# Performance work log

Hardware: AMD Instinct MI355X
Metric: run time of the kernel (lower is better)

## Reference

```python
import jax, jax.numpy as jnp
import numpy as np

N_NODES = 50000
N_EDGES = 800000
HIDDEN = 128
EDGE_DIM = 16
N_HEADS = 8
HEAD_DIM = HIDDEN // N_HEADS
SCALE = 1.0 / np.sqrt(HEAD_DIM).astype(np.float32)
LN_EPS = 1e-5


def setup_inputs() -> dict:
    key = jax.random.key(0)
    ks = jax.random.split(key, 24)
    s = 0.02

    def w(k, shape):
        return jax.random.normal(k, shape, dtype=jnp.float32) * s

    inp = {
        "node_features": jax.random.normal(ks[0], (N_NODES, HIDDEN), dtype=jnp.float32),
        "edge_index": jax.random.randint(ks[1], (2, N_EDGES), 0, N_NODES, dtype=jnp.int32),
        "edge_features": jax.random.normal(ks[2], (N_EDGES, EDGE_DIM), dtype=jnp.float32),
        # projections stored as [in, out] (y = x @ W + b)
        "Wq": w(ks[3], (HIDDEN, HIDDEN)), "bq": jnp.zeros((HIDDEN,), jnp.float32),
        "Wk": w(ks[4], (HIDDEN, HIDDEN)), "bk": jnp.zeros((HIDDEN,), jnp.float32),
        "Wv": w(ks[5], (HIDDEN, HIDDEN)), "bv": jnp.zeros((HIDDEN,), jnp.float32),
        "Wb1": w(ks[6], (EDGE_DIM, N_HEADS)), "bb1": jnp.zeros((N_HEADS,), jnp.float32),
        "Wb2": w(ks[7], (N_HEADS, N_HEADS)), "bb2": jnp.zeros((N_HEADS,), jnp.float32),
        "Wo": w(ks[8], (HIDDEN, HIDDEN)), "bo": jnp.zeros((HIDDEN,), jnp.float32),
        "Wf1": w(ks[9], (HIDDEN, 2 * HIDDEN)), "bf1": jnp.zeros((2 * HIDDEN,), jnp.float32),
        "Wf2": w(ks[10], (2 * HIDDEN, HIDDEN)), "bf2": jnp.zeros((HIDDEN,), jnp.float32),
        "g1": jnp.ones((HIDDEN,), jnp.float32), "be1": jnp.zeros((HIDDEN,), jnp.float32),
        "g2": jnp.ones((HIDDEN,), jnp.float32), "be2": jnp.zeros((HIDDEN,), jnp.float32),
    }
    return inp


def _layer_norm(x, gamma, beta):
    mu = jnp.mean(x, axis=-1, keepdims=True)
    var = jnp.mean(jnp.square(x - mu), axis=-1, keepdims=True)
    return (x - mu) * jax.lax.rsqrt(var + LN_EPS) * gamma + beta


def reference(node_features, edge_index, edge_features,
              Wq, bq, Wk, bk, Wv, bv, Wb1, bb1, Wb2, bb2,
              Wo, bo, Wf1, bf1, Wf2, bf2, g1, be1, g2, be2):
    n_nodes = node_features.shape[0]
    src, dst = edge_index[0], edge_index[1]

    q = (node_features @ Wq + bq).reshape(n_nodes, N_HEADS, HEAD_DIM)
    k = (node_features @ Wk + bk).reshape(n_nodes, N_HEADS, HEAD_DIM)
    v = (node_features @ Wv + bv).reshape(n_nodes, N_HEADS, HEAD_DIM)

    # per-edge attention logits [E, H]
    edge_bias = jax.nn.silu(edge_features @ Wb1 + bb1) @ Wb2 + bb2
    logits = jnp.sum(q[dst] * k[src], axis=-1) * SCALE + edge_bias

    # segment softmax over edges sharing the same dst node
    max_s = jax.ops.segment_max(logits, dst, num_segments=n_nodes)
    exp_s = jnp.exp(logits - max_s[dst])
    norm = jax.ops.segment_sum(exp_s, dst, num_segments=n_nodes)
    attn = exp_s / jnp.clip(norm[dst], 1e-12)

    # weighted aggregation [N, H, D] -> [N, hidden]
    weighted = attn[:, :, None] * v[src]
    aggregated = jax.ops.segment_sum(weighted, dst, num_segments=n_nodes)
    aggregated = aggregated.reshape(n_nodes, HIDDEN)

    x = _layer_norm(node_features + (aggregated @ Wo + bo), g1, be1)
    ffn = jax.nn.silu(x @ Wf1 + bf1) @ Wf2 + bf2
    return _layer_norm(x + ffn, g2, be2)
```

## Files before the change

kernel.cpp:

```cpp
#include <hip/hip_runtime.h>
#include <hip/hip_bf16.h>
#include <math.h>

#define HIDDEN 128
#define EDGE_DIM 16
#define N_HEADS 8
#define QK_SCALE 0.25f
#define LN_EPS 1e-5f
#define EB_SCALE 256.0f
#define EB_INV (1.0f / 256.0f)

using bf16x8 = __attribute__((ext_vector_type(8))) short;
using f32x4 = __attribute__((ext_vector_type(4))) float;
using f32x4v = __attribute__((ext_vector_type(4))) float;
using f32x2 = __attribute__((ext_vector_type(2))) float;
using i32x4 = __attribute__((ext_vector_type(4))) int;
typedef __hip_bfloat16 bf16;

__device__ __forceinline__ float b2f(short u) {
  union { unsigned int i; float f; } c;
  c.i = ((unsigned int)(unsigned short)u) << 16;
  return c.f;
}
__device__ __forceinline__ short f2b(float f) {
  bf16 h = __float2bfloat16(f);
  union { bf16 b; short s; } c;
  c.b = h;
  return c.s;
}
__device__ __forceinline__ unsigned char f2fp8(float f) {
  int pk = __builtin_amdgcn_cvt_pk_fp8_f32(f, f, 0, false);
  return (unsigned char)(pk & 0xff);
}

__global__ __launch_bounds__(256) void conv_weights_kernel(
    const float* __restrict__ Wq, const float* __restrict__ Wk, const float* __restrict__ Wv,
    const float* __restrict__ bq, const float* __restrict__ bk, const float* __restrict__ bv,
    const float* __restrict__ Wo, const float* __restrict__ Wf1, const float* __restrict__ Wf2,
    bf16* __restrict__ Wqkv_t, bf16* __restrict__ Wo_t, bf16* __restrict__ Wf1_t,
    bf16* __restrict__ Wf2_t, float* __restrict__ bqkv) {
  int i = blockIdx.x * 256 + threadIdx.x;
  if (i < 49152) {
    int n = i >> 7, k = i & 127;
    const float* W = (n < 128) ? Wq : ((n < 256) ? Wk : Wv);
    int nn = n & 127;
    Wqkv_t[i] = __float2bfloat16(W[k * 128 + nn]);
  } else if (i < 65536) {
    int j = i - 49152;
    int n = j >> 7, k = j & 127;
    Wo_t[j] = __float2bfloat16(Wo[k * 128 + n]);
  } else if (i < 98304) {
    int j = i - 65536;
    int n = j >> 7, k = j & 127;
    Wf1_t[j] = __float2bfloat16(Wf1[k * 256 + n]);
  } else if (i < 131072) {
    int j = i - 98304;
    int n = j >> 8, k = j & 255;
    Wf2_t[j] = __float2bfloat16(Wf2[k * 128 + n]);
  }
  if (i < 384) bqkv[i] = (i < 128) ? bq[i] : ((i < 256) ? bk[i - 128] : bv[i - 256]);
}

template <int K, int EPI, int OUTBF>
__global__ __launch_bounds__(256) void mfma_gemm_kernel(
    const bf16* __restrict__ A, const bf16* __restrict__ Wt,
    const float* __restrict__ bias, void* __restrict__ Cout, int M, int Nc) {
  const int tid = threadIdx.x;
  const int w = tid >> 6, l = tid & 63;
  const int wr = w >> 1, wc = w & 1;
  const int lr = l & 15, lk = l >> 4;
  const int bm = blockIdx.y * 64;
  const int bn = blockIdx.x * 128 + wc * 64;

  f32x4 acc[2][4] = {};
  const int arow0 = bm + wr * 32 + lr;

  for (int k0 = 0; k0 < K; k0 += 128) {
    bf16x8 bfr[4][4];
#pragma unroll
    for (int fn = 0; fn < 4; ++fn) {
      const bf16* wp = Wt + (size_t)(bn + fn * 16 + lr) * K + k0 + lk * 8;
#pragma unroll
      for (int ks = 0; ks < 4; ++ks) bfr[fn][ks] = *(const bf16x8*)(wp + ks * 32);
    }
    bf16x8 afr[2][4];
#pragma unroll
    for (int fr = 0; fr < 2; ++fr) {
      int row = arow0 + fr * 16;
      if (row >= M) row = M - 1;
      const bf16* ap = A + (size_t)row * K + k0 + lk * 8;
#pragma unroll
      for (int ks = 0; ks < 4; ++ks) afr[fr][ks] = *(const bf16x8*)(ap + ks * 32);
    }
#pragma unroll
    for (int ks = 0; ks < 4; ++ks)
#pragma unroll
      for (int fr = 0; fr < 2; ++fr)
#pragma unroll
        for (int fn = 0; fn < 4; ++fn)
          acc[fr][fn] = __builtin_amdgcn_mfma_f32_16x16x32_bf16(afr[fr][ks], bfr[fn][ks],
                                                                acc[fr][fn], 0, 0, 0);
  }

#pragma unroll
  for (int fn = 0; fn < 4; ++fn) {
    const int col = bn + fn * 16 + lr;
    const float bv = bias[col];
#pragma unroll
    for (int fr = 0; fr < 2; ++fr) {
      const int rbase = bm + wr * 32 + fr * 16 + lk * 4;
#pragma unroll
      for (int r = 0; r < 4; ++r) {
        int row = rbase + r;
        if (row < M) {
          float o = acc[fr][fn][r] + bv;
          if (EPI == 1) o = o / (1.f + __expf(-o));
          if (OUTBF)
            ((bf16*)Cout)[(size_t)row * Nc + col] = __float2bfloat16(o);
          else
            ((float*)Cout)[(size_t)row * Nc + col] = o;
        }
      }
    }
  }
}

__global__ __launch_bounds__(256) void mfma_gemm_qkv_kernel(
    const float* __restrict__ A, const bf16* __restrict__ Wt,
    const float* __restrict__ bias, bf16* __restrict__ qb,
    unsigned char* __restrict__ kv8, int M) {
  __shared__ __align__(16) char lds[64 * 272];
  const int tid = threadIdx.x;
  const int w = tid >> 6, l = tid & 63;
  const int wr = w >> 1, wc = w & 1;
  const int lr = l & 15, lk = l >> 4;
  const int bm = blockIdx.x * 64;
  const int arow0 = bm + wr * 32 + lr;

  bf16x8 afr[2][4];
#pragma unroll
  for (int fr = 0; fr < 2; ++fr) {
    int row = arow0 + fr * 16;
    if (row >= M) row = M - 1;
    const float* ap = A + (size_t)row * 128 + lk * 8;
#pragma unroll
    for (int ks = 0; ks < 4; ++ks) {
      float4 x = *(const float4*)(ap + ks * 32);
      float4 y = *(const float4*)(ap + ks * 32 + 4);
      bf16x8 t;
      t[0] = f2b(x.x); t[1] = f2b(x.y); t[2] = f2b(x.z); t[3] = f2b(x.w);
      t[4] = f2b(y.x); t[5] = f2b(y.y); t[6] = f2b(y.z); t[7] = f2b(y.w);
      afr[fr][ks] = t;
    }
  }

  const int row2 = tid >> 2, seg = tid & 3;
  const int grow = bm + row2;

#pragma unroll
  for (int s = 0; s < 3; ++s) {
    const int bn = s * 128 + wc * 64;
    bf16x8 bfr[4][4];
#pragma unroll
    for (int fn = 0; fn < 4; ++fn) {
      const bf16* wp = Wt + (size_t)(bn + fn * 16 + lr) * 128 + lk * 8;
#pragma unroll
      for (int ks = 0; ks < 4; ++ks) bfr[fn][ks] = *(const bf16x8*)(wp + ks * 32);
    }
    f32x4 acc[2][4] = {};
#pragma unroll
    for (int ks = 0; ks < 4; ++ks)
#pragma unroll
      for (int fr = 0; fr < 2; ++fr)
#pragma unroll
        for (int fn = 0; fn < 4; ++fn)
          acc[fr][fn] = __builtin_amdgcn_mfma_f32_16x16x32_bf16(afr[fr][ks], bfr[fn][ks],
                                                                acc[fr][fn], 0, 0, 0);

    if (s > 0) __syncthreads();
    if (s == 0) {
      short* sq = (short*)lds;
#pragma unroll
      for (int fn = 0; fn < 4; ++fn) {
        const int col = wc * 64 + fn * 16 + lr;
        const float bv = bias[bn + fn * 16 + lr];
#pragma unroll
        for (int fr = 0; fr < 2; ++fr) {
#pragma unroll
          for (int r = 0; r < 4; ++r) {
            int rl = wr * 32 + fr * 16 + lk * 4 + r;
            sq[rl * 136 + col] = f2b(acc[fr][fn][r] + bv);
          }
        }
      }
    } else {
      unsigned char* s8 = (unsigned char*)lds;
#pragma unroll
      for (int fn = 0; fn < 4; ++fn) {
        const int col = wc * 64 + fn * 16 + lr;
        const float bv = bias[bn + fn * 16 + lr];
#pragma unroll
        for (int fr = 0; fr < 2; ++fr) {
#pragma unroll
          for (int r = 0; r < 4; ++r) {
            int rl = wr * 32 + fr * 16 + lk * 4 + r;
            s8[rl * 144 + col] = f2fp8(acc[fr][fn][r] + bv);
          }
        }
      }
    }
    __syncthreads();

    if (grow < M) {
      if (s == 0) {
        const int4* src = (const int4*)(lds + row2 * 272 + seg * 64);
        int4* dst = (int4*)(qb + (size_t)grow * 128 + seg * 32);
        dst[0] = src[0];
        dst[1] = src[1];
        dst[2] = src[2];
        dst[3] = src[3];
      } else {
        const int4* src = (const int4*)(lds + row2 * 144 + seg * 32);
        int4* dst = (int4*)(kv8 + (size_t)grow * 256 + (s == 1 ? 0 : 128) + seg * 32);
        dst[0] = src[0];
        dst[1] = src[1];
      }
    }
  }
}

template <int K, int RBF>
__global__ __launch_bounds__(256) void mfma_gemm_ln_kernel(
    const bf16* __restrict__ A, const bf16* __restrict__ Wt,
    const float* __restrict__ bias, const void* __restrict__ Rp,
    const float* __restrict__ gam, const float* __restrict__ bet,
    float* __restrict__ y, bf16* __restrict__ yb, int M) {
  const int tid = threadIdx.x;
  const int w = tid >> 6, l = tid & 63;
  const int wr = w >> 1, wc = w & 1;
  const int lr = l & 15, lk = l >> 4;
  const int bm = blockIdx.x * 64;
  const int bn = wc * 64;

  f32x4 acc[2][4] = {};
  const int arow0 = bm + wr * 32 + lr;

  for (int k0 = 0; k0 < K; k0 += 128) {
    bf16x8 bfr[4][4];
#pragma unroll
    for (int fn = 0; fn < 4; ++fn) {
      const bf16* wp = Wt + (size_t)(bn + fn * 16 + lr) * K + k0 + lk * 8;
#pragma unroll
      for (int ks = 0; ks < 4; ++ks) bfr[fn][ks] = *(const bf16x8*)(wp + ks * 32);
    }
    bf16x8 afr[2][4];
#pragma unroll
    for (int fr = 0; fr < 2; ++fr) {
      int row = arow0 + fr * 16;
      if (row >= M) row = M - 1;
      const bf16* ap = A + (size_t)row * K + k0 + lk * 8;
#pragma unroll
      for (int ks = 0; ks < 4; ++ks) afr[fr][ks] = *(const bf16x8*)(ap + ks * 32);
    }
#pragma unroll
    for (int ks = 0; ks < 4; ++ks)
#pragma unroll
      for (int fr = 0; fr < 2; ++fr)
#pragma unroll
        for (int fn = 0; fn < 4; ++fn)
          acc[fr][fn] = __builtin_amdgcn_mfma_f32_16x16x32_bf16(afr[fr][ks], bfr[fn][ks],
                                                                acc[fr][fn], 0, 0, 0);
  }

  float bv[4], gv[4], ev[4];
#pragma unroll
  for (int fn = 0; fn < 4; ++fn) {
    int col = bn + fn * 16 + lr;
    bv[fn] = bias[col];
    gv[fn] = gam[col];
    ev[fn] = bet[col];
  }
  float ps[2][4], psq[2][4];
#pragma unroll
  for (int fr = 0; fr < 2; ++fr) {
#pragma unroll
    for (int r = 0; r < 4; ++r) {
      int row = bm + wr * 32 + fr * 16 + lk * 4 + r;
      int rrow = (row < M) ? row : (M - 1);
      float s = 0.f, sq = 0.f;
#pragma unroll
      for (int fn = 0; fn < 4; ++fn) {
        int col = bn + fn * 16 + lr;
        float rv;
        if (RBF)
          rv = b2f(((const short*)Rp)[(size_t)rrow * HIDDEN + col]);
        else
          rv = ((const float*)Rp)[(size_t)rrow * HIDDEN + col];
        float o = acc[fr][fn][r] + bv[fn] + rv;
        acc[fr][fn][r] = o;
        s += o;
        sq += o * o;
      }
      ps[fr][r] = s;
      psq[fr][r] = sq;
    }
  }
#pragma unroll
  for (int off = 1; off < 16; off <<= 1) {
#pragma unroll
    for (int fr = 0; fr < 2; ++fr)
#pragma unroll
      for (int r = 0; r < 4; ++r) {
        ps[fr][r] += __shfl_xor(ps[fr][r], off, 64);
        psq[fr][r] += __shfl_xor(psq[fr][r], off, 64);
      }
  }
  __shared__ float s_sum[2][64], s_sq[2][64];
  if (lr == 0) {
#pragma unroll
    for (int fr = 0; fr < 2; ++fr)
#pragma unroll
      for (int r = 0; r < 4; ++r) {
        int rl = wr * 32 + fr * 16 + lk * 4 + r;
        s_sum[wc][rl] = ps[fr][r];
        s_sq[wc][rl] = psq[fr][r];
      }
  }
  __syncthreads();
#pragma unroll
  for (int fr = 0; fr < 2; ++fr) {
#pragma unroll
    for (int r = 0; r < 4; ++r) {
      int rl = wr * 32 + fr * 16 + lk * 4 + r;
      int row = bm + rl;
      float tot = s_sum[0][rl] + s_sum[1][rl];
      float tsq = s_sq[0][rl] + s_sq[1][rl];
      float mean = tot * (1.f / 128.f);
      float var = tsq * (1.f / 128.f) - mean * mean;
      float rstd = rsqrtf(var + LN_EPS);
      if (row < M) {
#pragma unroll
        for (int fn = 0; fn < 4; ++fn) {
          int col = bn + fn * 16 + lr;
          float val = (acc[fr][fn][r] - mean) * rstd * gv[fn] + ev[fn];
          if (y) y[(size_t)row * HIDDEN + col] = val;
          if (yb) yb[(size_t)row * HIDDEN + col] = __float2bfloat16(val);
        }
      }
    }
  }
}

__global__ void hist_kernel(const int* __restrict__ dst, int* __restrict__ counts, int E) {
  int e = blockIdx.x * blockDim.x + threadIdx.x;
  if (e < E) atomicAdd(&counts[dst[e]], 1);
}

__device__ __forceinline__ int wave_incl_scan(int x, int lane) {
  int incl = x;
#pragma unroll
  for (int off = 1; off < 64; off <<= 1) {
    int y = __shfl_up(incl, off, 64);
    if (lane >= off) incl += y;
  }
  return incl;
}

__global__ __launch_bounds__(256) void scan_block_kernel(const int* __restrict__ counts,
                                                         int* __restrict__ offs,
                                                         int* __restrict__ btot, int N) {
  __shared__ int s4[4];
  int tid = threadIdx.x;
  int i = blockIdx.x * 256 + tid;
  int lane = tid & 63, wv = tid >> 6;
  int x = (i < N) ? counts[i] : 0;
  int incl = wave_incl_scan(x, lane);
  if (lane == 63) s4[wv] = incl;
  __syncthreads();
  if (tid == 0) {
    int s = 0;
#pragma unroll
    for (int j = 0; j < 4; ++j) { int t = s4[j]; s4[j] = s; s += t; }
    btot[blockIdx.x] = s;
  }
  __syncthreads();
  if (i < N) offs[i] = s4[wv] + incl - x;
}

__global__ __launch_bounds__(256) void scan_tot_kernel(int* __restrict__ btot, int nb) {
  __shared__ int s4[4];
  __shared__ int carry;
  int tid = threadIdx.x;
  int lane = tid & 63, wv = tid >> 6;
  if (tid == 0) carry = 0;
  __syncthreads();
  for (int c0 = 0; c0 < nb; c0 += 256) {
    int i = c0 + tid;
    int x = (i < nb) ? btot[i] : 0;
    int incl = wave_incl_scan(x, lane);
    if (lane == 63) s4[wv] = incl;
    __syncthreads();
    if (tid == 0) {
      int s = 0;
#pragma unroll
      for (int j = 0; j < 4; ++j) { int t = s4[j]; s4[j] = s; s += t; }
    }
    __syncthreads();
    int base = carry + s4[wv];
    if (i < nb) btot[i] = base + incl - x;
    __syncthreads();
    if (tid == 255) carry = base + incl;
    __syncthreads();
  }
}

__global__ __launch_bounds__(256) void scan_add_kernel(int* __restrict__ offs,
                                                       const int* __restrict__ btot,
                                                       int N, int E) {
  int i = blockIdx.x * 256 + threadIdx.x;
  if (i < N) offs[i] += btot[blockIdx.x];
  if (i == 0) offs[N] = E;
}

__global__ __launch_bounds__(256) void scatter_mlp_kernel(
    const int* __restrict__ dst, const int* __restrict__ src,
    const float* __restrict__ ef, const float* __restrict__ Wb1,
    const float* __restrict__ bb1, const float* __restrict__ Wb2,
    const float* __restrict__ bb2, const int* __restrict__ offs,
    int* __restrict__ cursor, i32x4* __restrict__ es16, int E) {
  __shared__ float w1[128], w2[64], b1[8], b2[8];
  int tid = threadIdx.x;
  if (tid < 128) w1[tid] = Wb1[tid];
  else if (tid < 192) w2[tid - 128] = Wb2[tid - 128];
  else if (tid < 200) b1[tid - 192] = bb1[tid - 192];
  else if (tid < 208) b2[tid - 200] = bb2[tid - 200];
  __syncthreads();

  int e = blockIdx.x * 256 + tid;
  if (e >= E) return;

  const f32x4v* p4 = (const f32x4v*)(ef + (size_t)e * 16);
  f32x4v f0 = __builtin_nontemporal_load(p4 + 0);
  f32x4v f1 = __builtin_nontemporal_load(p4 + 1);
  f32x4v f2 = __builtin_nontemporal_load(p4 + 2);
  f32x4v f3 = __builtin_nontemporal_load(p4 + 3);
  float x[16] = {f0[0], f0[1], f0[2], f0[3], f1[0], f1[1], f1[2], f1[3],
                 f2[0], f2[1], f2[2], f2[3], f3[0], f3[1], f3[2], f3[3]};

  float h[8];
#pragma unroll
  for (int j = 0; j < 8; ++j) h[j] = b1[j];
#pragma unroll
  for (int i = 0; i < 16; ++i) {
    float xi = x[i];
#pragma unroll
    for (int j = 0; j < 8; ++j) h[j] = fmaf(xi, w1[i * 8 + j], h[j]);
  }
#pragma unroll
  for (int j = 0; j < 8; ++j) h[j] = h[j] / (1.f + __expf(-h[j]));

  float o[8];
#pragma unroll
  for (int j = 0; j < 8; ++j) o[j] = b2[j];
#pragma unroll
  for (int jj = 0; jj < 8; ++jj) {
    float hj = h[jj];
#pragma unroll
    for (int j = 0; j < 8; ++j) o[j] = fmaf(hj, w2[jj * 8 + j], o[j]);
  }

  int lo = __builtin_amdgcn_cvt_pk_fp8_f32(o[0] * EB_SCALE, o[1] * EB_SCALE, 0, false);
  lo = __builtin_amdgcn_cvt_pk_fp8_f32(o[2] * EB_SCALE, o[3] * EB_SCALE, lo, true);
  int hi = __builtin_amdgcn_cvt_pk_fp8_f32(o[4] * EB_SCALE, o[5] * EB_SCALE, 0, false);
  hi = __builtin_amdgcn_cvt_pk_fp8_f32(o[6] * EB_SCALE, o[7] * EB_SCALE, hi, true);

  int d = dst[e];
  int p = offs[d] + atomicAdd(&cursor[d], 1);
  i32x4 rec;
  rec[0] = src[e]; rec[1] = lo; rec[2] = hi; rec[3] = 0;
  es16[p] = rec;
}

__global__ __launch_bounds__(256) void node_attn_kernel(
    const bf16* __restrict__ qb, const unsigned char* __restrict__ kv8,
    const i32x4* __restrict__ es16, const int* __restrict__ offs,
    bf16* __restrict__ agg, int Nn) {
  int n = blockIdx.x * 4 + (threadIdx.x >> 6);
  if (n >= Nn) return;
  int l = threadIdx.x & 63;
  int g = l >> 3;
  int il = l & 7;

  int s0 = offs[n], s1 = offs[n + 1];
  bf16* orow = agg + (size_t)n * HIDDEN + il * 16;
  if (s0 >= s1) {
    if (g == 0) {
      bf16x8 z = {};
      *(bf16x8*)(orow) = z;
      *(bf16x8*)(orow + 8) = z;
    }
    return;
  }

  const bf16* qrow = qb + (size_t)n * 128 + il * 16;
  bf16x8 qa = *(const bf16x8*)(qrow);
  bf16x8 qb8 = *(const bf16x8*)(qrow + 8);
  float qf[16];
#pragma unroll
  for (int j = 0; j < 8; ++j) {
    qf[j] = b2f(qa[j]) * QK_SCALE;
    qf[8 + j] = b2f(qb8[j]) * QK_SCALE;
  }

  float lsum = 0.f;
  float acc[16] = {};
  const int ebshift = (il & 2) << 3;

  for (int p0 = s0; p0 < s1; p0 += 8) {
    int p = p0 + g;
    bool valid = p < s1;
    int pc = valid ? p : s1 - 1;
    i32x4 rec = es16[pc];
    int cs = rec[0];
    unsigned ebw = (unsigned)((il < 4) ? rec[1] : rec[2]);
    f32x2 ebp = __builtin_amdgcn_cvt_pk_f32_fp8(ebw >> ebshift, false);
    float ebv = ((il & 1) ? ebp[1] : ebp[0]) * EB_INV;

    const unsigned char* kvrow = kv8 + (size_t)cs * 256 + il * 16;
    i32x4 kw = *(const i32x4*)(kvrow);
    i32x4 vw = *(const i32x4*)(kvrow + 128);

    float prod = 0.f;
#pragma unroll
    for (int w2 = 0; w2 < 4; ++w2) {
      f32x2 lo = __builtin_amdgcn_cvt_pk_f32_fp8(kw[w2], false);
      f32x2 hi = __builtin_amdgcn_cvt_pk_f32_fp8(kw[w2], true);
      prod = fmaf(qf[w2 * 4 + 0], lo[0], prod);
      prod = fmaf(qf[w2 * 4 + 1], lo[1], prod);
      prod = fmaf(qf[w2 * 4 + 2], hi[0], prod);
      prod = fmaf(qf[w2 * 4 + 3], hi[1], prod);
    }
    float pe = valid ? __expf(prod + ebv) : 0.f;
    lsum += pe;
#pragma unroll
    for (int w2 = 0; w2 < 4; ++w2) {
      f32x2 lo = __builtin_amdgcn_cvt_pk_f32_fp8(vw[w2], false);
      f32x2 hi = __builtin_amdgcn_cvt_pk_f32_fp8(vw[w2], true);
      acc[w2 * 4 + 0] = fmaf(pe, lo[0], acc[w2 * 4 + 0]);
      acc[w2 * 4 + 1] = fmaf(pe, lo[1], acc[w2 * 4 + 1]);
      acc[w2 * 4 + 2] = fmaf(pe, hi[0], acc[w2 * 4 + 2]);
      acc[w2 * 4 + 3] = fmaf(pe, hi[1], acc[w2 * 4 + 3]);
    }
  }

#pragma unroll
  for (int off = 8; off < 64; off <<= 1) {
    lsum += __shfl_xor(lsum, off, 64);
#pragma unroll
    for (int j = 0; j < 16; ++j) acc[j] += __shfl_xor(acc[j], off, 64);
  }

  if (g == 0) {
    float inv = (lsum > 0.f) ? 1.f / lsum : 0.f;
    bf16x8 o0, o1;
#pragma unroll
    for (int j = 0; j < 8; ++j) {
      o0[j] = f2b(acc[j] * inv);
      o1[j] = f2b(acc[8 + j] * inv);
    }
    *(bf16x8*)(orow) = o0;
    *(bf16x8*)(orow + 8) = o1;
  }
}

extern "C" void kernel_launch(void* const* d_in, const int* in_sizes, int n_in,
                              void* d_out, int out_size, void* d_ws, size_t ws_size,
                              hipStream_t stream) {
  const float* nf = (const float*)d_in[0];
  const int* ei = (const int*)d_in[1];
  const float* ef = (const float*)d_in[2];
  const float* Wq = (const float*)d_in[3];
  const float* bq = (const float*)d_in[4];
  const float* Wk = (const float*)d_in[5];
  const float* bk_ = (const float*)d_in[6];
  const float* Wv = (const float*)d_in[7];
  const float* bv = (const float*)d_in[8];
  const float* Wb1 = (const float*)d_in[9];
  const float* bb1 = (const float*)d_in[10];
  const float* Wb2 = (const float*)d_in[11];
  const float* bb2 = (const float*)d_in[12];
  const float* Wo = (const float*)d_in[13];
  const float* bo = (const float*)d_in[14];
  const float* Wf1 = (const float*)d_in[15];
  const float* bf1 = (const float*)d_in[16];
  const float* Wf2 = (const float*)d_in[17];
  const float* bf2 = (const float*)d_in[18];
  const float* g1 = (const float*)d_in[19];
  const float* be1 = (const float*)d_in[20];
  const float* g2 = (const float*)d_in[21];
  const float* be2 = (const float*)d_in[22];

  const int N = in_sizes[0] / HIDDEN;
  const int E = in_sizes[2] / EDGE_DIM;
  const int* srcA = ei;
  const int* dstA = ei + E;

  char* base = (char*)d_ws;
  size_t off = 0;
  auto alloc = [&](size_t bytes) {
    off = (off + 255) & ~(size_t)255;
    char* p = base + off;
    off += bytes;
    return p;
  };

  size_t qb_bytes = (size_t)N * 128 * 2;
  size_t kv_bytes = (size_t)N * 256;
  size_t hb_bytes = (size_t)N * 256 * 2;
  char* regB = alloc(hb_bytes > qb_bytes + kv_bytes ? hb_bytes : qb_bytes + kv_bytes);
  bf16* qb = (bf16*)regB;
  unsigned char* kv8 = (unsigned char*)(regB + qb_bytes);
  bf16* hbuf = (bf16*)regB;
  bf16* agg = (bf16*)alloc((size_t)N * HIDDEN * 2);
  bf16* x1b = (bf16*)alloc((size_t)N * HIDDEN * 2);
  i32x4* es16 = (i32x4*)alloc((size_t)E * 16);
  int* counts = (int*)alloc((size_t)N * 8);
  int* cursor = counts + N;
  int* offs = (int*)alloc((size_t)(N + 1) * 4);
  const int nb = (N + 255) / 256;
  int* btot = (int*)alloc((size_t)nb * 4);
  bf16* Wqkv_t = (bf16*)alloc(384 * 128 * 2);
  bf16* Wo_t = (bf16*)alloc(128 * 128 * 2);
  bf16* Wf1_t = (bf16*)alloc(256 * 128 * 2);
  bf16* Wf2_t = (bf16*)alloc(128 * 256 * 2);
  float* bqkv = (float*)alloc(384 * 4);

  float* outp = (float*)d_out;
  const int mb64 = (N + 63) / 64;
  const int eblocks = (E + 255) / 256;

  conv_weights_kernel<<<512, 256, 0, stream>>>(Wq, Wk, Wv, bq, bk_, bv, Wo, Wf1, Wf2,
                                               Wqkv_t, Wo_t, Wf1_t, Wf2_t, bqkv);

  mfma_gemm_qkv_kernel<<<mb64, 256, 0, stream>>>(nf, Wqkv_t, bqkv, qb, kv8, N);

  hipMemsetAsync(counts, 0, (size_t)N * 8, stream);
  hist_kernel<<<eblocks, 256, 0, stream>>>(dstA, counts, E);
  scan_block_kernel<<<nb, 256, 0, stream>>>(counts, offs, btot, N);
  scan_tot_kernel<<<1, 256, 0, stream>>>(btot, nb);
  scan_add_kernel<<<nb, 256, 0, stream>>>(offs, btot, N, E);
  scatter_mlp_kernel<<<eblocks, 256, 0, stream>>>(dstA, srcA, ef, Wb1, bb1, Wb2, bb2,
                                                  offs, cursor, es16, E);

  node_attn_kernel<<<(N + 3) / 4, 256, 0, stream>>>(qb, kv8, es16, offs, agg, N);

  mfma_gemm_ln_kernel<128, 0><<<mb64, 256, 0, stream>>>(agg, Wo_t, bo, nf, g1, be1,
                                                        nullptr, x1b, N);

  mfma_gemm_kernel<128, 1, 1><<<dim3(2, mb64), 256, 0, stream>>>(
      x1b, Wf1_t, bf1, hbuf, N, 256);

  mfma_gemm_ln_kernel<256, 1><<<mb64, 256, 0, stream>>>(hbuf, Wf2_t, bf2, x1b, g2, be2,
                                                        outp, nullptr, N);
}
```

Baseline: 265.3 us.

## Split edge MLP from CSR scatter and place edge ids in dst-bucketed passes

The edge-bias MLP now writes 16-byte records in edge order with coalesced nontemporal stores. A separate placement kernel runs 8 passes over the edges, each handling only destinations in one address band, and writes 4-byte edge ids into CSR order. A gather kernel then copies the records into CSR order. The aim is to replace random 16-byte scattered stores and scattered atomics with more localized atomics and smaller scattered writes. The cost is an extra full read and write of the edge records, 8 reads of dst, and two more launches.

```diff
diff --git a/kernel.cpp b/kernel.cpp
--- a/kernel.cpp
+++ b/kernel.cpp
@@ -422,12 +422,11 @@
   if (i == 0) offs[N] = E;
 }
 
-__global__ __launch_bounds__(256) void scatter_mlp_kernel(
-    const int* __restrict__ dst, const int* __restrict__ src,
-    const float* __restrict__ ef, const float* __restrict__ Wb1,
-    const float* __restrict__ bb1, const float* __restrict__ Wb2,
-    const float* __restrict__ bb2, const int* __restrict__ offs,
-    int* __restrict__ cursor, i32x4* __restrict__ es16, int E) {
+__global__ __launch_bounds__(256) void mlp_seq_kernel(
+    const int* __restrict__ src, const float* __restrict__ ef,
+    const float* __restrict__ Wb1, const float* __restrict__ bb1,
+    const float* __restrict__ Wb2, const float* __restrict__ bb2,
+    i32x4* __restrict__ es_seq, int E) {
   __shared__ float w1[128], w2[64], b1[8], b2[8];
   int tid = threadIdx.x;
   if (tid < 128) w1[tid] = Wb1[tid];
@@ -474,11 +473,32 @@
   int hi = __builtin_amdgcn_cvt_pk_fp8_f32(o[4] * EB_SCALE, o[5] * EB_SCALE, 0, false);
   hi = __builtin_amdgcn_cvt_pk_fp8_f32(o[6] * EB_SCALE, o[7] * EB_SCALE, hi, true);
 
-  int d = dst[e];
-  int p = offs[d] + atomicAdd(&cursor[d], 1);
   i32x4 rec;
   rec[0] = src[e]; rec[1] = lo; rec[2] = hi; rec[3] = 0;
-  es16[p] = rec;
+  __builtin_nontemporal_store(rec, es_seq + e);
+}
+
+__global__ __launch_bounds__(256) void place8_kernel(
+    const int* __restrict__ dst, const int* __restrict__ offs,
+    int* __restrict__ cursor, int* __restrict__ eid_csr, int E) {
+  int bid = blockIdx.x;
+  int chunk = bid >> 3;
+  int want = bid & 7;
+  int e = chunk * 256 + threadIdx.x;
+  if (e >= E) return;
+  int d = dst[e];
+  if (((d >> 5) & 7) != want) return;
+  int p = offs[d] + atomicAdd(&cursor[d], 1);
+  eid_csr[p] = e;
+}
+
+__global__ __launch_bounds__(256) void gather_place_kernel(
+    const i32x4* __restrict__ es_seq, const int* __restrict__ eid_csr,
+    i32x4* __restrict__ es16, int E) {
+  int p = blockIdx.x * 256 + threadIdx.x;
+  if (p >= E) return;
+  i32x4 rec = es_seq[eid_csr[p]];
+  __builtin_nontemporal_store(rec, es16 + p);
 }
 
 __global__ __launch_bounds__(256) void node_attn_kernel(
@@ -623,7 +643,9 @@
   bf16* hbuf = (bf16*)regB;
   bf16* agg = (bf16*)alloc((size_t)N * HIDDEN * 2);
   bf16* x1b = (bf16*)alloc((size_t)N * HIDDEN * 2);
+  i32x4* es_seq = (i32x4*)alloc((size_t)E * 16);
   i32x4* es16 = (i32x4*)alloc((size_t)E * 16);
+  int* eid_csr = (int*)alloc((size_t)E * 4);
   int* counts = (int*)alloc((size_t)N * 8);
   int* cursor = counts + N;
   int* offs = (int*)alloc((size_t)(N + 1) * 4);
@@ -644,13 +666,16 @@
 
   mfma_gemm_qkv_kernel<<<mb64, 256, 0, stream>>>(nf, Wqkv_t, bqkv, qb, kv8, N);
 
+  mlp_seq_kernel<<<eblocks, 256, 0, stream>>>(srcA, ef, Wb1, bb1, Wb2, bb2, es_seq, E);
+
   hipMemsetAsync(counts, 0, (size_t)N * 8, stream);
   hist_kernel<<<eblocks, 256, 0, stream>>>(dstA, counts, E);
   scan_block_kernel<<<nb, 256, 0, stream>>>(counts, offs, btot, N);
   scan_tot_kernel<<<1, 256, 0, stream>>>(btot, nb);
   scan_add_kernel<<<nb, 256, 0, stream>>>(offs, btot, N, E);
-  scatter_mlp_kernel<<<eblocks, 256, 0, stream>>>(dstA, srcA, ef, Wb1, bb1, Wb2, bb2,
-                                                  offs, cursor, es16, E);
+
+  place8_kernel<<<eblocks * 8, 256, 0, stream>>>(dstA, offs, cursor, eid_csr, E);
+  gather_place_kernel<<<eblocks, 256, 0, stream>>>(es_seq, eid_csr, es16, E);
 
   node_attn_kernel<<<(N + 3) / 4, 256, 0, stream>>>(qb, kv8, es16, offs, agg, N);
 
```

After: 288.3 us. 8.6% more time.
